# Kernel tuning notes

Measured on AMD Instinct MI355X. Metric: run time of the kernel, lower is better.

Reference implementation:

```python
import jax, jax.numpy as jnp
import numpy as np

B, N, D, BS = 2, 4096, 2048, 256  # batch, seq, d_model, chunk size


def rms_norm(x):
    eps = jnp.asarray(jnp.finfo(x.dtype).eps, x.dtype)
    return x * jax.lax.rsqrt(jnp.mean(x * x, axis=-1, keepdims=True) + eps)


def la_kernel(q, k, v, bs):
    # chunked linear attention: intra-chunk masked QK^T + cross-chunk KV recurrence
    b, n, d = q.shape
    T = n // bs
    qc = q.reshape(b, T, bs, d).transpose(1, 0, 2, 3)  # [T,B,bs,d]
    kc = k.reshape(b, T, bs, d).transpose(1, 0, 2, 3)
    vc = v.reshape(b, T, bs, d).transpose(1, 0, 2, 3)
    mask = jnp.tril(jnp.ones((bs, bs), q.dtype))

    def step(kv, qkv):
        qt, kt, vt = qkv  # each [B,bs,d]
        s = jnp.einsum('bid,bjd->bij', qt, kt) * mask        # masked intra-chunk scores
        ot = jnp.einsum('bij,bjd->bid', s, vt) + jnp.einsum('bid,bde->bie', qt, kv)
        kv = kv + jnp.einsum('bjd,bje->bde', kt, vt)          # state update AFTER output
        return kv, ot

    kv0 = jnp.zeros((b, d, d), q.dtype)
    _, o = jax.lax.scan(step, kv0, (qc, kc, vc))              # o: [T,B,bs,d]
    return o.transpose(1, 0, 2, 3).reshape(b, n, d)


def setup_inputs() -> dict:
    key = jax.random.key(0)
    ks = jax.random.split(key, 6)
    scale = 0.02
    x = jax.random.normal(ks[0], (B, N, D), jnp.float32)
    Wq = jax.random.normal(ks[1], (D, D), jnp.float32) * scale
    Wk = jax.random.normal(ks[2], (D, D), jnp.float32) * scale
    Wv = jax.random.normal(ks[3], (D, D), jnp.float32) * scale
    Wg = jax.random.normal(ks[4], (D, D), jnp.float32) * scale
    Wp = jax.random.normal(ks[5], (D, D), jnp.float32) * scale
    return {'x': x, 'Wq': Wq, 'Wk': Wk, 'Wv': Wv, 'Wg': Wg, 'Wp': Wp}


def reference(x, Wq, Wk, Wv, Wg, Wp):
    # weights stored torch-style (out,in): y = x @ W^T
    xn = rms_norm(x)
    q = jax.nn.silu(jnp.einsum('bnd,od->bno', xn, Wq))
    k = jax.nn.silu(jnp.einsum('bnd,od->bno', xn, Wk))
    v = jax.nn.silu(jnp.einsum('bnd,od->bno', xn, Wv))
    g = jax.nn.sigmoid(jnp.einsum('bnd,od->bno', xn, Wg))
    o = la_kernel(q, k, v, BS) * g
    return jnp.einsum('bnd,od->bno', o, Wp)
```

## Files before the change

### kernel.cpp

```cpp
#include <hip/hip_runtime.h>
#include <hip/hip_bf16.h>

typedef __bf16 bf16;
typedef __bf16 bf16x8 __attribute__((ext_vector_type(8)));
typedef float f32x4 __attribute__((ext_vector_type(4)));
typedef unsigned int u32;

#define D_    2048
#define NSEQ  4096
#define BATCH 2
#define CH    1024
#define TC    4
#define MROWS 8192

__device__ __forceinline__ void gload16(const bf16* g, bf16* l) {
  __builtin_amdgcn_global_load_lds(
      (const __attribute__((address_space(1))) u32*)g,
      (__attribute__((address_space(3))) u32*)l, 16, 0, 0);
}


struct SmemTiles {
  alignas(16) bf16 As[2][128 * 32];
  alignas(16) bf16 Bs[2][128 * 32];
};

__device__ __forceinline__ void stage128(SmemTiles& sm, int bb, const bf16* A,
                                         int lda, const bf16* B, int ldb,
                                         int k0, int tid) {
#pragma unroll
  for (int it = 0; it < 2; ++it) {
    int c = it * 256 + tid;
    int r = c >> 2;
    int co = (c & 3) << 3;
    gload16(A + (size_t)r * lda + k0 + co, &sm.As[bb][c * 8]);
    gload16(B + (size_t)r * ldb + k0 + co, &sm.Bs[bb][c * 8]);
  }
}

__device__ __forceinline__ void gemm_core(SmemTiles& sm, const bf16* A, int lda,
                                          const bf16* B, int ldb, int K,
                                          f32x4 acc[4][4]) {
  const int tid = threadIdx.x;
  const int lane = tid & 63;
  const int wave = tid >> 6;
  const int wr = wave >> 1, wc = wave & 1;
  const int l15 = lane & 15, kl = lane >> 4;
  const int NT = K >> 5;
  if (NT <= 0) return;

  stage128(sm, 0, A, lda, B, ldb, 0, tid);
  __syncthreads();

  const int ao = (wr * 64 + l15) * 32 + kl * 8;
  const int bo = (wc * 64 + l15) * 32 + kl * 8;

  for (int t = 0; t < NT; ++t) {
    if (t + 1 < NT)
      stage128(sm, (t + 1) & 1, A, lda, B, ldb, (t + 1) * 32, tid);
    const bf16* Ab = sm.As[t & 1];
    const bf16* Bb = sm.Bs[t & 1];
    bf16x8 a[4], b[4];
#pragma unroll
    for (int m = 0; m < 4; ++m) a[m] = *(const bf16x8*)(Ab + ao + m * 16 * 32);
#pragma unroll
    for (int n = 0; n < 4; ++n) b[n] = *(const bf16x8*)(Bb + bo + n * 16 * 32);
    __builtin_amdgcn_s_setprio(1);
#pragma unroll
    for (int m = 0; m < 4; ++m)
#pragma unroll
      for (int n = 0; n < 4; ++n)
        acc[m][n] = __builtin_amdgcn_mfma_f32_16x16x32_bf16(a[m], b[n], acc[m][n], 0, 0, 0);
    __builtin_amdgcn_s_setprio(0);
    if (t + 1 < NT) __syncthreads();
  }
}

#define EPILOGUE_VARS                              \
  const int lane = threadIdx.x & 63;               \
  const int wave = threadIdx.x >> 6;               \
  const int wr = wave >> 1, wc = wave & 1;         \
  const int l15 = lane & 15, kl = lane >> 4;


struct SmemW {
  alignas(16) bf16 A[2][128 * 32];
  alignas(16) bf16 B[2][256 * 32];
};

__device__ __forceinline__ void stageW(SmemW& sm, int bb, const bf16* A,
                                       int lda, const bf16* B, int ldb,
                                       int k0, int wave, int lane) {
  const int r16 = lane & 15, c8 = lane >> 4;
  gload16(A + (size_t)(wave * 16 + r16) * lda + k0 + c8 * 8,
          &sm.A[bb][wave * 512 + lane * 8]);
#pragma unroll
  for (int j = 0; j < 2; ++j) {
    int nb = 2 * wave + j;
    gload16(B + (size_t)(nb * 16 + r16) * ldb + k0 + c8 * 8,
            &sm.B[bb][nb * 512 + lane * 8]);
  }
}

__device__ __forceinline__ void gemmW_core(SmemW& sm, const bf16* A, int lda,
                                           const bf16* B, int ldb, int K,
                                           f32x4 acc[4][4]) {
  const int tid = threadIdx.x;
  const int wave = tid >> 6, lane = tid & 63;
  const int wr = wave >> 2, wc = wave & 3;
  const int NT = K >> 5;
  if (NT <= 0) return;

  stageW(sm, 0, A, lda, B, ldb, 0, wave, lane);
  if (NT > 1) {
    stageW(sm, 1, A, lda, B, ldb, 32, wave, lane);
    asm volatile("s_waitcnt vmcnt(3)" ::: "memory");
  } else {
    asm volatile("s_waitcnt vmcnt(0)" ::: "memory");
  }
  __builtin_amdgcn_s_barrier();

  const int aoff = wr * 2048 + lane * 8;
  const int boff = wc * 2048 + lane * 8;

  for (int t = 0; t < NT; ++t) {
    const bf16* Ab = sm.A[t & 1];
    const bf16* Bb = sm.B[t & 1];
    bf16x8 av[4], bv[4];
#pragma unroll
    for (int m = 0; m < 4; ++m) av[m] = *(const bf16x8*)&Ab[aoff + m * 512];
#pragma unroll
    for (int n = 0; n < 4; ++n) bv[n] = *(const bf16x8*)&Bb[boff + n * 512];
    asm volatile("s_waitcnt lgkmcnt(0)" ::: "memory");
    __builtin_amdgcn_s_barrier();
    if (t + 2 < NT)
      stageW(sm, t & 1, A, lda, B, ldb, (t + 2) * 32, wave, lane);
    __builtin_amdgcn_s_setprio(1);
#pragma unroll
    for (int m = 0; m < 4; ++m)
#pragma unroll
      for (int n = 0; n < 4; ++n)
        acc[m][n] = __builtin_amdgcn_mfma_f32_16x16x32_bf16(av[m], bv[n],
                                                            acc[m][n], 0, 0, 0);
    __builtin_amdgcn_s_setprio(0);
    if (t + 1 < NT) {
      if (t + 2 < NT)
        asm volatile("s_waitcnt vmcnt(3)" ::: "memory");
      else
        asm volatile("s_waitcnt vmcnt(0)" ::: "memory");
      __builtin_amdgcn_s_barrier();
    }
  }
}

#define EPILOGUEW_VARS                             \
  const int lane = threadIdx.x & 63;               \
  const int wave = threadIdx.x >> 6;               \
  const int wr = wave >> 2, wc = wave & 3;         \
  const int l15 = lane & 15, kl = lane >> 4;


__global__ __launch_bounds__(256) void k_f2b(const float* __restrict__ in,
                                             bf16* __restrict__ out) {
  int i = (blockIdx.x * 256 + threadIdx.x) * 8;
  float4 a = *(const float4*)(in + i);
  float4 b = *(const float4*)(in + i + 4);
  bf16x8 o;
  o[0] = (bf16)a.x; o[1] = (bf16)a.y; o[2] = (bf16)a.z; o[3] = (bf16)a.w;
  o[4] = (bf16)b.x; o[5] = (bf16)b.y; o[6] = (bf16)b.z; o[7] = (bf16)b.w;
  *(bf16x8*)(out + i) = o;
}

__global__ __launch_bounds__(256) void k_f2b2(const float* __restrict__ in0,
                                              const float* __restrict__ in1,
                                              bf16* __restrict__ out) {
  int i = (blockIdx.x * 256 + threadIdx.x) * 8;
  const float* src = (i < D_ * D_) ? in0 : in1;
  int off = (i < D_ * D_) ? i : i - D_ * D_;
  float4 a = *(const float4*)(src + off);
  float4 b = *(const float4*)(src + off + 4);
  bf16x8 o;
  o[0] = (bf16)a.x; o[1] = (bf16)a.y; o[2] = (bf16)a.z; o[3] = (bf16)a.w;
  o[4] = (bf16)b.x; o[5] = (bf16)b.y; o[6] = (bf16)b.z; o[7] = (bf16)b.w;
  *(bf16x8*)(out + i) = o;
}

__global__ __launch_bounds__(256) void k_rms(const float* __restrict__ x,
                                             bf16* __restrict__ xn) {
  const int row = blockIdx.x;
  const int tid = threadIdx.x;
  const float* xr = x + (size_t)row * D_;
  float4 a = *(const float4*)(xr + tid * 8);
  float4 b = *(const float4*)(xr + tid * 8 + 4);
  float ss = a.x * a.x + a.y * a.y + a.z * a.z + a.w * a.w +
             b.x * b.x + b.y * b.y + b.z * b.z + b.w * b.w;
#pragma unroll
  for (int o = 32; o > 0; o >>= 1) ss += __shfl_xor(ss, o, 64);
  __shared__ float red[4];
  if ((tid & 63) == 0) red[tid >> 6] = ss;
  __syncthreads();
  float tot = red[0] + red[1] + red[2] + red[3];
  float sc = rsqrtf(tot * (1.f / D_) + 1.1920928955078125e-07f);
  bf16x8 o;
  o[0] = (bf16)(a.x * sc); o[1] = (bf16)(a.y * sc);
  o[2] = (bf16)(a.z * sc); o[3] = (bf16)(a.w * sc);
  o[4] = (bf16)(b.x * sc); o[5] = (bf16)(b.y * sc);
  o[6] = (bf16)(b.z * sc); o[7] = (bf16)(b.w * sc);
  *(bf16x8*)(xn + (size_t)row * D_ + tid * 8) = o;
}


template <int ACT, int SMODE>
__global__ __launch_bounds__(512, 4) void k_proj2(const bf16* __restrict__ xn,
                                                  const bf16* __restrict__ W,
                                                  bf16* __restrict__ Cn,
                                                  bf16* __restrict__ Ct) {
  __shared__ SmemW sm;
  const int row0 = blockIdx.y * 128, col0 = blockIdx.x * 256;
  f32x4 acc[4][4] = {};
  gemmW_core(sm, xn + (size_t)row0 * D_, D_, W + (size_t)col0 * D_, D_, D_, acc);
  EPILOGUEW_VARS
#pragma unroll
  for (int m = 0; m < 4; ++m)
#pragma unroll
    for (int n = 0; n < 4; ++n)
#pragma unroll
      for (int j = 0; j < 4; ++j) {
        int r = row0 + wr * 64 + m * 16 + kl * 4 + j;
        int c = col0 + wc * 64 + n * 16 + l15;
        float v = acc[m][n][j];
        if (ACT == 1) v = v / (1.f + __expf(-v));
        if (ACT == 2) v = 1.f / (1.f + __expf(-v));
        bf16 ob = (bf16)v;
        if (SMODE & 1) Cn[(size_t)r * D_ + c] = ob;
        if (SMODE & 2)
          Ct[((size_t)(r >> 12) * D_ + c) * NSEQ + (r & (NSEQ - 1))] = ob;
      }
}

__global__ __launch_bounds__(512, 4) void k_final2(const bf16* __restrict__ og,
                                                   const bf16* __restrict__ Wp,
                                                   float* __restrict__ out) {
  __shared__ SmemW sm;
  const int row0 = blockIdx.y * 128, col0 = blockIdx.x * 256;
  f32x4 acc[4][4] = {};
  gemmW_core(sm, og + (size_t)row0 * D_, D_, Wp + (size_t)col0 * D_, D_, D_, acc);
  EPILOGUEW_VARS
#pragma unroll
  for (int m = 0; m < 4; ++m)
#pragma unroll
    for (int n = 0; n < 4; ++n)
#pragma unroll
      for (int j = 0; j < 4; ++j) {
        int r = row0 + wr * 64 + m * 16 + kl * 4 + j;
        int c = col0 + wc * 64 + n * 16 + l15;
        out[(size_t)r * D_ + c] = acc[m][n][j];
      }
}


__global__ __launch_bounds__(256) void k_scores(const bf16* __restrict__ q,
                                                const bf16* __restrict__ k,
                                                bf16* __restrict__ s) {
  const int z = blockIdx.z, b = z >> 2, t = z & 3;
  const int row0 = blockIdx.y * 128, col0 = blockIdx.x * 128;
  if (col0 > row0) return;
  __shared__ SmemTiles sm;
  f32x4 acc[4][4] = {};
  gemm_core(sm, q + (size_t)(b * NSEQ + t * CH + row0) * D_, D_,
                k + (size_t)(b * NSEQ + t * CH + col0) * D_, D_, D_, acc);
  EPILOGUE_VARS
  bf16* sp = s + (size_t)z * CH * CH;
#pragma unroll
  for (int m = 0; m < 4; ++m)
#pragma unroll
    for (int n = 0; n < 4; ++n)
#pragma unroll
      for (int j = 0; j < 4; ++j) {
        int i = row0 + wr * 64 + m * 16 + kl * 4 + j;
        int jc = col0 + wc * 64 + n * 16 + l15;
        float v = (i >= jc) ? acc[m][n][j] : 0.f;
        sp[(size_t)i * CH + jc] = (bf16)v;
      }
}

__global__ __launch_bounds__(256) void k_ointra(const bf16* __restrict__ s,
                                                const bf16* __restrict__ vT,
                                                bf16* __restrict__ og) {
  __shared__ SmemTiles sm;
  const int z = blockIdx.z, b = z >> 2, t = z & 3;
  const int row0 = blockIdx.y * 128, col0 = blockIdx.x * 128;
  const int K = row0 + 128;
  f32x4 acc[4][4] = {};
  gemm_core(sm, s + (size_t)z * CH * CH + (size_t)row0 * CH, CH,
                vT + (size_t)b * D_ * NSEQ + (size_t)col0 * NSEQ + t * CH, NSEQ,
                K, acc);
  EPILOGUE_VARS
#pragma unroll
  for (int m = 0; m < 4; ++m)
#pragma unroll
    for (int n = 0; n < 4; ++n)
#pragma unroll
      for (int j = 0; j < 4; ++j) {
        int i = row0 + wr * 64 + m * 16 + kl * 4 + j;
        int c = col0 + wc * 64 + n * 16 + l15;
        og[(size_t)(b * NSEQ + t * CH + i) * D_ + c] = (bf16)acc[m][n][j];
      }
}

__global__ __launch_bounds__(256) void k_ointer(const bf16* __restrict__ q,
                                                const bf16* __restrict__ kvb,
                                                const bf16* __restrict__ g,
                                                bf16* __restrict__ og, int t,
                                                int Kin) {
  __shared__ SmemTiles sm;
  const int b = blockIdx.z;
  const int row0 = blockIdx.y * 128, col0 = blockIdx.x * 128;
  f32x4 acc[4][4] = {};
  gemm_core(sm, q + (size_t)(b * NSEQ + t * CH + row0) * D_, D_,
                kvb + (size_t)b * D_ * D_ + (size_t)col0 * D_, D_, Kin, acc);
  EPILOGUE_VARS
#pragma unroll
  for (int m = 0; m < 4; ++m)
#pragma unroll
    for (int n = 0; n < 4; ++n)
#pragma unroll
      for (int j = 0; j < 4; ++j) {
        int i = row0 + wr * 64 + m * 16 + kl * 4 + j;
        int c = col0 + wc * 64 + n * 16 + l15;
        size_t idx = (size_t)(b * NSEQ + t * CH + i) * D_ + c;
        float v = ((float)og[idx] + acc[m][n][j]) * (float)g[idx];
        og[idx] = (bf16)v;
      }
}

__global__ __launch_bounds__(256) void k_update(const bf16* __restrict__ vT,
                                                const bf16* __restrict__ kT,
                                                bf16* __restrict__ kvb, int t) {
  __shared__ SmemTiles sm;
  const int b = blockIdx.z;
  const int row0 = blockIdx.y * 128, col0 = blockIdx.x * 128;
  f32x4 acc[4][4] = {};
  gemm_core(sm, vT + (size_t)b * D_ * NSEQ + (size_t)row0 * NSEQ + t * CH, NSEQ,
                kT + (size_t)b * D_ * NSEQ + (size_t)col0 * NSEQ + t * CH, NSEQ,
                CH, acc);
  EPILOGUE_VARS
#pragma unroll
  for (int m = 0; m < 4; ++m)
#pragma unroll
    for (int n = 0; n < 4; ++n)
#pragma unroll
      for (int j = 0; j < 4; ++j) {
        int e = row0 + wr * 64 + m * 16 + kl * 4 + j;
        int d = col0 + wc * 64 + n * 16 + l15;
        size_t idx = (size_t)b * D_ * D_ + (size_t)e * D_ + d;
        float v = acc[m][n][j];
        if (t > 0) v += (float)kvb[idx];
        kvb[idx] = (bf16)v;
      }
}


extern "C" void kernel_launch(void* const* d_in, const int* in_sizes, int n_in,
                              void* d_out, int out_size, void* d_ws, size_t ws_size,
                              hipStream_t stream) {
  (void)in_sizes; (void)n_in; (void)out_size; (void)ws_size;
  const float* x  = (const float*)d_in[0];
  const float* Wq = (const float*)d_in[1];
  const float* Wk = (const float*)d_in[2];
  const float* Wv = (const float*)d_in[3];
  const float* Wg = (const float*)d_in[4];
  const float* Wp = (const float*)d_in[5];
  float* out = (float*)d_out;

  char* p = (char*)d_ws;
  auto take = [&](size_t bytes) {
    char* r = p;
    p += (bytes + 255) & ~(size_t)255;
    return r;
  };
  const size_t MD2 = (size_t)MROWS * D_ * 2;

  bf16* xn  = (bf16*)take(MD2);
  bf16* kT  = (bf16*)take(MD2);
  bf16* vT  = (bf16*)take(MD2);
  bf16* k   = (bf16*)take((size_t)MROWS * D_ * 2);
  char* shared = take((size_t)BATCH * TC * CH * CH * 2);
  bf16* Wpair = (bf16*)shared;
  bf16* s    = (bf16*)shared;
  bf16* kvb  = (bf16*)shared;
  bf16* og = xn;

  bf16* q = (bf16*)d_out;
  bf16* g = (bf16*)d_out + (size_t)MROWS * D_;

  const size_t W1 = (size_t)D_ * D_;
  dim3 gpW(D_ / 256, MROWS / 128);

  k_rms<<<MROWS, 256, 0, stream>>>(x, xn);

  k_f2b2<<<2 * (D_ * D_) / 2048, 256, 0, stream>>>(Wq, Wk, Wpair);
  k_proj2<1, 1><<<gpW, 512, 0, stream>>>(xn, Wpair, q, (bf16*)nullptr);
  k_proj2<1, 3><<<gpW, 512, 0, stream>>>(xn, Wpair + W1, k, kT);
  k_f2b2<<<2 * (D_ * D_) / 2048, 256, 0, stream>>>(Wv, Wg, Wpair);
  k_proj2<1, 2><<<gpW, 512, 0, stream>>>(xn, Wpair, (bf16*)nullptr, vT);
  k_proj2<2, 1><<<gpW, 512, 0, stream>>>(xn, Wpair + W1, g, (bf16*)nullptr);

  k_scores<<<dim3(CH / 128, CH / 128, BATCH * TC), 256, 0, stream>>>(q, k, s);
  k_ointra<<<dim3(D_ / 128, CH / 128, BATCH * TC), 256, 0, stream>>>(s, vT, og);

  for (int t = 0; t < TC; ++t) {
    k_ointer<<<dim3(D_ / 128, CH / 128, BATCH), 256, 0, stream>>>(
        q, kvb, g, og, t, t ? D_ : 0);
    if (t < TC - 1)
      k_update<<<dim3(D_ / 128, D_ / 128, BATCH), 256, 0, stream>>>(vT, kT,
                                                                    kvb, t);
  }

  bf16* Wpb = (bf16*)shared;
  k_f2b<<<(D_ * D_) / 2048, 256, 0, stream>>>(Wp, Wpb);
  k_final2<<<gpW, 512, 0, stream>>>(og, Wpb, out);
}
```

Baseline: 872.4 us.

## Skip empty first inter-chunk pass, swizzle GEMM blocks across XCDs, vectorize transposed stores

The first chunk's inter-chunk GEMM had a zero-length K loop and existed only to apply the gate. That launch is removed and the gate is folded into the intra-chunk epilogue for t==0. The projection and final GEMMs remap block indices so that blocks sharing the same rows land on the same XCD, which should improve L2 reuse. The transposed store in the projection epilogue is vectorized to 4-wide bf16 writes. The block remap hardcodes an 8x64 grid split and assumes 8 XCDs.

```diff
diff --git a/kernel.cpp b/kernel.cpp
--- a/kernel.cpp
+++ b/kernel.cpp
@@ -2,6 +2,7 @@
 #include <hip/hip_bf16.h>
 
 typedef __bf16 bf16;
+typedef __bf16 bf16x4 __attribute__((ext_vector_type(4)));
 typedef __bf16 bf16x8 __attribute__((ext_vector_type(8)));
 typedef float f32x4 __attribute__((ext_vector_type(4)));
 typedef unsigned int u32;
@@ -158,6 +159,13 @@
   const int wave = threadIdx.x >> 6;               \
   const int wr = wave >> 2, wc = wave & 3;         \
   const int l15 = lane & 15, kl = lane >> 4;
+
+__device__ __forceinline__ void swzW(int& bx, int& by) {
+  int lin = blockIdx.y * gridDim.x + blockIdx.x;
+  int xcd = lin & 7, pos = lin >> 3;
+  by = xcd * 8 + (pos >> 3);
+  bx = pos & 7;
+}
 
 
 __global__ __launch_bounds__(256) void k_f2b(const float* __restrict__ in,
@@ -216,33 +224,44 @@
                                                   bf16* __restrict__ Cn,
                                                   bf16* __restrict__ Ct) {
   __shared__ SmemW sm;
-  const int row0 = blockIdx.y * 128, col0 = blockIdx.x * 256;
+  int bx, by;
+  swzW(bx, by);
+  const int row0 = by * 128, col0 = bx * 256;
   f32x4 acc[4][4] = {};
   gemmW_core(sm, xn + (size_t)row0 * D_, D_, W + (size_t)col0 * D_, D_, D_, acc);
   EPILOGUEW_VARS
 #pragma unroll
   for (int m = 0; m < 4; ++m)
 #pragma unroll
-    for (int n = 0; n < 4; ++n)
-#pragma unroll
-      for (int j = 0; j < 4; ++j) {
-        int r = row0 + wr * 64 + m * 16 + kl * 4 + j;
-        int c = col0 + wc * 64 + n * 16 + l15;
+    for (int n = 0; n < 4; ++n) {
+      const int rb = row0 + wr * 64 + m * 16 + kl * 4;
+      const int c = col0 + wc * 64 + n * 16 + l15;
+      bf16 ob[4];
+#pragma unroll
+      for (int j = 0; j < 4; ++j) {
         float v = acc[m][n][j];
         if (ACT == 1) v = v / (1.f + __expf(-v));
         if (ACT == 2) v = 1.f / (1.f + __expf(-v));
-        bf16 ob = (bf16)v;
-        if (SMODE & 1) Cn[(size_t)r * D_ + c] = ob;
-        if (SMODE & 2)
-          Ct[((size_t)(r >> 12) * D_ + c) * NSEQ + (r & (NSEQ - 1))] = ob;
-      }
+        ob[j] = (bf16)v;
+      }
+      if (SMODE & 1) {
+#pragma unroll
+        for (int j = 0; j < 4; ++j) Cn[(size_t)(rb + j) * D_ + c] = ob[j];
+      }
+      if (SMODE & 2) {
+        bf16x4 tv = {ob[0], ob[1], ob[2], ob[3]};
+        *(bf16x4*)&Ct[((size_t)(rb >> 12) * D_ + c) * NSEQ + (rb & (NSEQ - 1))] = tv;
+      }
+    }
 }
 
 __global__ __launch_bounds__(512, 4) void k_final2(const bf16* __restrict__ og,
                                                    const bf16* __restrict__ Wp,
                                                    float* __restrict__ out) {
   __shared__ SmemW sm;
-  const int row0 = blockIdx.y * 128, col0 = blockIdx.x * 256;
+  int bx, by;
+  swzW(bx, by);
+  const int row0 = by * 128, col0 = bx * 256;
   f32x4 acc[4][4] = {};
   gemmW_core(sm, og + (size_t)row0 * D_, D_, Wp + (size_t)col0 * D_, D_, D_, acc);
   EPILOGUEW_VARS
@@ -286,6 +305,7 @@
 
 __global__ __launch_bounds__(256) void k_ointra(const bf16* __restrict__ s,
                                                 const bf16* __restrict__ vT,
+                                                const bf16* __restrict__ g,
                                                 bf16* __restrict__ og) {
   __shared__ SmemTiles sm;
   const int z = blockIdx.z, b = z >> 2, t = z & 3;
@@ -296,6 +316,7 @@
                 vT + (size_t)b * D_ * NSEQ + (size_t)col0 * NSEQ + t * CH, NSEQ,
                 K, acc);
   EPILOGUE_VARS
+  const bool gate0 = (t == 0);
 #pragma unroll
   for (int m = 0; m < 4; ++m)
 #pragma unroll
@@ -304,21 +325,23 @@
       for (int j = 0; j < 4; ++j) {
         int i = row0 + wr * 64 + m * 16 + kl * 4 + j;
         int c = col0 + wc * 64 + n * 16 + l15;
-        og[(size_t)(b * NSEQ + t * CH + i) * D_ + c] = (bf16)acc[m][n][j];
+        size_t idx = (size_t)(b * NSEQ + t * CH + i) * D_ + c;
+        float v = acc[m][n][j];
+        if (gate0) v *= (float)g[idx];
+        og[idx] = (bf16)v;
       }
 }
 
 __global__ __launch_bounds__(256) void k_ointer(const bf16* __restrict__ q,
                                                 const bf16* __restrict__ kvb,
                                                 const bf16* __restrict__ g,
-                                                bf16* __restrict__ og, int t,
-                                                int Kin) {
+                                                bf16* __restrict__ og, int t) {
   __shared__ SmemTiles sm;
   const int b = blockIdx.z;
   const int row0 = blockIdx.y * 128, col0 = blockIdx.x * 128;
   f32x4 acc[4][4] = {};
   gemm_core(sm, q + (size_t)(b * NSEQ + t * CH + row0) * D_, D_,
-                kvb + (size_t)b * D_ * D_ + (size_t)col0 * D_, D_, Kin, acc);
+                kvb + (size_t)b * D_ * D_ + (size_t)col0 * D_, D_, D_, acc);
   EPILOGUE_VARS
 #pragma unroll
   for (int m = 0; m < 4; ++m)
@@ -407,14 +430,13 @@
   k_proj2<2, 1><<<gpW, 512, 0, stream>>>(xn, Wpair + W1, g, (bf16*)nullptr);
 
   k_scores<<<dim3(CH / 128, CH / 128, BATCH * TC), 256, 0, stream>>>(q, k, s);
-  k_ointra<<<dim3(D_ / 128, CH / 128, BATCH * TC), 256, 0, stream>>>(s, vT, og);
-
-  for (int t = 0; t < TC; ++t) {
-    k_ointer<<<dim3(D_ / 128, CH / 128, BATCH), 256, 0, stream>>>(
-        q, kvb, g, og, t, t ? D_ : 0);
-    if (t < TC - 1)
-      k_update<<<dim3(D_ / 128, D_ / 128, BATCH), 256, 0, stream>>>(vT, kT,
-                                                                    kvb, t);
+  k_ointra<<<dim3(D_ / 128, CH / 128, BATCH * TC), 256, 0, stream>>>(s, vT, g, og);
+
+  for (int t = 1; t < TC; ++t) {
+    k_update<<<dim3(D_ / 128, D_ / 128, BATCH), 256, 0, stream>>>(vT, kT,
+                                                                  kvb, t - 1);
+    k_ointer<<<dim3(D_ / 128, CH / 128, BATCH), 256, 0, stream>>>(q, kvb, g,
+                                                                  og, t);
   }
 
   bf16* Wpb = (bf16*)shared;
```

New measurement: 847.0 us. -2.9%, faster.
